# Kernel optimization log

Hardware: AMD Instinct MI355X
Metric: run time of the kernel (lower is better)

The kernel has to match this reference:

```python
import jax, jax.numpy as jnp
import numpy as np

TEMPERATURE = 0.07  # module init default
CHUNK = 2048        # row tile size, mirrors the triton tiling (never materialize full NxN)


def _normalize(x):
    # F.normalize(x, dim=1): x / max(||x||_2, eps)
    n = jnp.linalg.norm(x, axis=1, keepdims=True)
    return x / jnp.maximum(n, 1e-12)


def setup_inputs() -> dict:
    key = jax.random.key(0)
    k1, k2 = jax.random.split(key)
    N, D = 16384, 256
    return {
        "text_features": jax.random.normal(k1, (N, D), dtype=jnp.float32),
        "image_features": jax.random.normal(k2, (N, D), dtype=jnp.float32),
    }


def reference(text_features, image_features):
    X = _normalize(text_features)   # [N, D]
    Y = _normalize(image_features)  # [N, D]
    inv_t = 1.0 / TEMPERATURE
    n, d = X.shape
    Xc = X.reshape(n // CHUNK, CHUNK, d)

    def row_sum_exp(xc):
        # exp2(S*log2(e)/t - log2(e)/t) == exp((S - 1)/t); S = xc @ Y^T
        S = (jnp.einsum('id,jd->ij', xc, Y) - 1.0) * inv_t  # [CHUNK, N]
        return jnp.sum(jnp.exp(S), axis=1)                   # [CHUNK]

    # tiled accumulation of row-wise sum of exponentials (never holds NxN)
    sum_exp_row = jax.lax.map(row_sum_exp, Xc).reshape(n)   # [N]

    # diagonal (positive-pair) logits: Sv = (x_i . y_i - 1)/t
    Sv = (jnp.sum(X * Y, axis=1) - 1.0) * inv_t
    logits = jnp.log(jnp.exp(Sv) / sum_exp_row)
    return -jnp.mean(logits)
```

## Files before the change

### kernel.cpp

```cpp
#include <hip/hip_runtime.h>
#include <hip/hip_bf16.h>
#include <stdint.h>

#define D_DIM 256
#define INV_T 14.285714285714286f

#define BM 256
#define BN 256
#define BK 64
#define NSTEP (D_DIM / BK)

typedef __bf16 bf16x8 __attribute__((ext_vector_type(8)));
typedef float f32x16 __attribute__((ext_vector_type(16)));

__global__ __launch_bounds__(256) void lit_normalize(
    const float* __restrict__ X, const float* __restrict__ Y,
    __hip_bfloat16* __restrict__ Xb, __hip_bfloat16* __restrict__ Yb,
    float* __restrict__ Sv, float* __restrict__ rowsum, float* __restrict__ acc1)
{
    const int l = threadIdx.x & 63;
    const int row = blockIdx.x * 4 + (threadIdx.x >> 6);
    const size_t base = (size_t)row * D_DIM;
    const float4 x = ((const float4*)(X + base))[l];
    const float4 y = ((const float4*)(Y + base))[l];
    float nx = x.x * x.x + x.y * x.y + x.z * x.z + x.w * x.w;
    float ny = y.x * y.x + y.y * y.y + y.z * y.z + y.w * y.w;
    float dt = x.x * y.x + x.y * y.y + x.z * y.z + x.w * y.w;
    #pragma unroll
    for (int o = 1; o < 64; o <<= 1) {
        nx += __shfl_xor(nx, o);
        ny += __shfl_xor(ny, o);
        dt += __shfl_xor(dt, o);
    }
    const float ivx = 1.0f / fmaxf(sqrtf(nx), 1e-12f);
    const float ivy = 1.0f / fmaxf(sqrtf(ny), 1e-12f);

    __hip_bfloat16 hx0 = __float2bfloat16(x.x * ivx), hx1 = __float2bfloat16(x.y * ivx);
    __hip_bfloat16 hx2 = __float2bfloat16(x.z * ivx), hx3 = __float2bfloat16(x.w * ivx);
    __hip_bfloat16 hy0 = __float2bfloat16(y.x * ivy), hy1 = __float2bfloat16(y.y * ivy);
    __hip_bfloat16 hy2 = __float2bfloat16(y.z * ivy), hy3 = __float2bfloat16(y.w * ivy);
    ushort4 px, py;
    px.x = *(unsigned short*)&hx0; px.y = *(unsigned short*)&hx1;
    px.z = *(unsigned short*)&hx2; px.w = *(unsigned short*)&hx3;
    py.x = *(unsigned short*)&hy0; py.y = *(unsigned short*)&hy1;
    py.z = *(unsigned short*)&hy2; py.w = *(unsigned short*)&hy3;
    ((ushort4*)(Xb + base))[l] = px;
    ((ushort4*)(Yb + base))[l] = py;

    if (l == 0) {
        Sv[row] = (dt * ivx * ivy - 1.0f) * INV_T;
        rowsum[row] = 0.0f;
    }
    if (blockIdx.x == 0 && threadIdx.x == 0) acc1[0] = 0.0f;
}

__global__ __launch_bounds__(512, 2) void lit_gemm_rowsum(
    const __hip_bfloat16* __restrict__ Xb, const __hip_bfloat16* __restrict__ Yb,
    float* __restrict__ rowsum)
{
    __shared__ char lds[BM * BK * 2 + BN * BK * 2];

    const int tid = (int)threadIdx.x;
    const int l   = tid & 63;
    const int w   = tid >> 6;
    const int wi  = w >> 2;
    const int wj  = w & 3;

    const int nx  = (int)gridDim.x;
    const int bid = (int)blockIdx.y * nx + (int)blockIdx.x;
    const int cpx = (nx * (int)gridDim.y) >> 3;
    const int logical = (bid & 7) * cpx + (bid >> 3);
    const int bi = logical / nx;
    const int bj = logical % nx;
    const int iBase = bi * BM;
    const int jBase = bj * BN;

    f32x16 acc[2][4];
    #pragma unroll
    for (int a = 0; a < 2; ++a)
        #pragma unroll
        for (int b = 0; b < 4; ++b)
            #pragma unroll
            for (int r = 0; r < 16; ++r)
                acc[a][b][r] = 0.f;

    const int rq = l >> 3;
    const int sl = l & 7;
    const char* src[8];
    int dst[8];
    #pragma unroll
    for (int c = 0; c < 8; ++c) {
        const int g    = w * 8 + c;
        const int isY  = g >> 5;
        const int r8   = (g & 31) * 8;
        const int row  = r8 + rq;
        const int slot = sl ^ (row & 7);
        const char* base = isY ? (const char*)Yb + (size_t)jBase * (D_DIM * 2)
                               : (const char*)Xb + (size_t)iBase * (D_DIM * 2);
        src[c] = base + (size_t)row * (D_DIM * 2) + slot * 16;
        dst[c] = isY * (BM * BK * 2) + r8 * 128;
    }

    #pragma unroll
    for (int t = 0; t < NSTEP; ++t) {
        #pragma unroll
        for (int c = 0; c < 8; ++c)
            __builtin_amdgcn_global_load_lds(
                (const __attribute__((address_space(1))) void*)(src[c] + t * (BK * 2)),
                (__attribute__((address_space(3))) void*)(lds + dst[c]),
                16, 0, 0);
        __syncthreads();

        const char* Xs = lds;
        const char* Ys = lds + BM * BK * 2;
        #pragma unroll
        for (int kk = 0; kk < 4; ++kk) {
            const int sx = ((kk * 2 + (l >> 5)) ^ (l & 7)) * 16;
            const int lr = l & 31;
            bf16x8 a0 = *(const bf16x8*)(Ys + (wj * 64 +  0 + lr) * 128 + sx);
            bf16x8 a1 = *(const bf16x8*)(Ys + (wj * 64 + 32 + lr) * 128 + sx);
            bf16x8 b0 = *(const bf16x8*)(Xs + (wi * 128 +  0 + lr) * 128 + sx);
            bf16x8 b1 = *(const bf16x8*)(Xs + (wi * 128 + 32 + lr) * 128 + sx);
            bf16x8 b2 = *(const bf16x8*)(Xs + (wi * 128 + 64 + lr) * 128 + sx);
            bf16x8 b3 = *(const bf16x8*)(Xs + (wi * 128 + 96 + lr) * 128 + sx);
            acc[0][0] = __builtin_amdgcn_mfma_f32_32x32x16_bf16(a0, b0, acc[0][0], 0, 0, 0);
            acc[0][1] = __builtin_amdgcn_mfma_f32_32x32x16_bf16(a0, b1, acc[0][1], 0, 0, 0);
            acc[0][2] = __builtin_amdgcn_mfma_f32_32x32x16_bf16(a0, b2, acc[0][2], 0, 0, 0);
            acc[0][3] = __builtin_amdgcn_mfma_f32_32x32x16_bf16(a0, b3, acc[0][3], 0, 0, 0);
            acc[1][0] = __builtin_amdgcn_mfma_f32_32x32x16_bf16(a1, b0, acc[1][0], 0, 0, 0);
            acc[1][1] = __builtin_amdgcn_mfma_f32_32x32x16_bf16(a1, b1, acc[1][1], 0, 0, 0);
            acc[1][2] = __builtin_amdgcn_mfma_f32_32x32x16_bf16(a1, b2, acc[1][2], 0, 0, 0);
            acc[1][3] = __builtin_amdgcn_mfma_f32_32x32x16_bf16(a1, b3, acc[1][3], 0, 0, 0);
        }
        __syncthreads();
    }

    float part[4];
    #pragma unroll
    for (int fi = 0; fi < 4; ++fi) {
        float s = 0.f;
        #pragma unroll
        for (int fj = 0; fj < 2; ++fj)
            #pragma unroll
            for (int r = 0; r < 16; ++r)
                s += __expf(fmaf(acc[fj][fi][r], INV_T, -INV_T));
        s += __shfl_xor(s, 32);
        part[fi] = s;
    }
    float* rowpart = (float*)lds;
    if (tid < BM) rowpart[tid] = 0.f;
    __syncthreads();
    if (l < 32) {
        #pragma unroll
        for (int fi = 0; fi < 4; ++fi)
            atomicAdd(&rowpart[wi * 128 + fi * 32 + l], part[fi]);
    }
    __syncthreads();
    if (tid < BM) atomicAdd(&rowsum[iBase + tid], rowpart[tid]);
}

__global__ __launch_bounds__(256) void lit_partial(
    const float* __restrict__ Sv, const float* __restrict__ rowsum,
    float* __restrict__ acc1)
{
    const int i = blockIdx.x * 256 + threadIdx.x;
    float v = Sv[i] - logf(rowsum[i]);
    #pragma unroll
    for (int o = 1; o < 64; o <<= 1) v += __shfl_xor(v, o);
    __shared__ float sred[4];
    if ((threadIdx.x & 63) == 0) sred[threadIdx.x >> 6] = v;
    __syncthreads();
    if (threadIdx.x == 0)
        atomicAdd(acc1, sred[0] + sred[1] + sred[2] + sred[3]);
}

__global__ void lit_final(const float* __restrict__ acc1, float* __restrict__ out, int N)
{
    out[0] = -acc1[0] / (float)N;
}

extern "C" void kernel_launch(void* const* d_in, const int* in_sizes, int n_in,
                              void* d_out, int out_size, void* d_ws, size_t ws_size,
                              hipStream_t stream)
{
    const float* X = (const float*)d_in[0];
    const float* Y = (const float*)d_in[1];
    const int N = in_sizes[0] / D_DIM;

    char* ws = (char*)d_ws;
    __hip_bfloat16* Xb = (__hip_bfloat16*)ws;
    __hip_bfloat16* Yb = (__hip_bfloat16*)(ws + (size_t)N * D_DIM * 2);
    float* Sv     = (float*)(ws + (size_t)N * D_DIM * 4);
    float* rowsum = (float*)(ws + (size_t)N * D_DIM * 4 + (size_t)N * 4);
    float* acc1   = (float*)(ws + (size_t)N * D_DIM * 4 + (size_t)N * 8);

    lit_normalize<<<N / 4, 256, 0, stream>>>(X, Y, Xb, Yb, Sv, rowsum, acc1);
    dim3 grid(N / BN, N / BM);
    lit_gemm_rowsum<<<grid, 512, 0, stream>>>(Xb, Yb, rowsum);
    lit_partial<<<N / 256, 256, 0, stream>>>(Sv, rowsum, acc1);
    lit_final<<<1, 1, 0, stream>>>(acc1, (float*)d_out, N);
}
```

Measured before the change: 265.5 us.

## Double-buffer GEMM K tiles with async LDS loads and fuse final reduction

Cuts the K tile to 32 and double-buffers LDS so the global-to-LDS load of the next tile overlaps the MFMAs on the current one, using explicit vmcnt waits and raw barriers, with a new swizzle for the 64-byte rows. It raises wave priority around the MFMA bursts. It also drops the partial and final kernels by having the last finishing GEMM block, found through an atomic counter, compute the log-sum mean. This saves two launches but adds a serial tail reduction done by one block.

```diff
diff --git a/kernel.cpp b/kernel.cpp
--- a/kernel.cpp
+++ b/kernel.cpp
@@ -7,7 +7,7 @@
 
 #define BM 256
 #define BN 256
-#define BK 64
+#define BK 32
 #define NSTEP (D_DIM / BK)
 
 typedef __bf16 bf16x8 __attribute__((ext_vector_type(8)));
@@ -16,7 +16,7 @@
 __global__ __launch_bounds__(256) void lit_normalize(
     const float* __restrict__ X, const float* __restrict__ Y,
     __hip_bfloat16* __restrict__ Xb, __hip_bfloat16* __restrict__ Yb,
-    float* __restrict__ Sv, float* __restrict__ rowsum, float* __restrict__ acc1)
+    float* __restrict__ Sv, float* __restrict__ rowsum, unsigned* __restrict__ done)
 {
     const int l = threadIdx.x & 63;
     const int row = blockIdx.x * 4 + (threadIdx.x >> 6);
@@ -51,14 +51,15 @@
         Sv[row] = (dt * ivx * ivy - 1.0f) * INV_T;
         rowsum[row] = 0.0f;
     }
-    if (blockIdx.x == 0 && threadIdx.x == 0) acc1[0] = 0.0f;
+    if (blockIdx.x == 0 && threadIdx.x == 0) done[0] = 0u;
 }
 
 __global__ __launch_bounds__(512, 2) void lit_gemm_rowsum(
     const __hip_bfloat16* __restrict__ Xb, const __hip_bfloat16* __restrict__ Yb,
-    float* __restrict__ rowsum)
+    const float* __restrict__ Sv, float* __restrict__ rowsum,
+    unsigned* __restrict__ done, float* __restrict__ out, int N)
 {
-    __shared__ char lds[BM * BK * 2 + BN * BK * 2];
+    __shared__ char lds[2 * 32768];
 
     const int tid = (int)threadIdx.x;
     const int l   = tid & 63;
@@ -84,45 +85,59 @@
             for (int r = 0; r < 16; ++r)
                 acc[a][b][r] = 0.f;
 
-    const int rq = l >> 3;
-    const int sl = l & 7;
-    const char* src[8];
-    int dst[8];
-    #pragma unroll
-    for (int c = 0; c < 8; ++c) {
-        const int g    = w * 8 + c;
-        const int isY  = g >> 5;
-        const int r8   = (g & 31) * 8;
-        const int row  = r8 + rq;
-        const int slot = sl ^ (row & 7);
+    const int rq = l >> 2;
+    const int sl = l & 3;
+    const char* src[4];
+    int dst[4];
+    #pragma unroll
+    for (int c = 0; c < 4; ++c) {
+        const int g    = w * 4 + c;
+        const int isY  = g >> 4;
+        const int r16  = (g & 15) * 16;
+        const int row  = r16 + rq;
+        const int slot = sl ^ ((row >> 1) & 3);
         const char* base = isY ? (const char*)Yb + (size_t)jBase * (D_DIM * 2)
                                : (const char*)Xb + (size_t)iBase * (D_DIM * 2);
         src[c] = base + (size_t)row * (D_DIM * 2) + slot * 16;
-        dst[c] = isY * (BM * BK * 2) + r8 * 128;
-    }
+        dst[c] = isY * 16384 + r16 * 64;
+    }
+
+#define STAGE(buf, t)                                                              \
+    {                                                                              \
+        _Pragma("unroll")                                                          \
+        for (int c = 0; c < 4; ++c)                                                \
+            __builtin_amdgcn_global_load_lds(                                      \
+                (const __attribute__((address_space(1))) void*)(src[c] + (t) * (BK * 2)), \
+                (__attribute__((address_space(3))) void*)(lds + (buf) * 32768 + dst[c]),  \
+                16, 0, 0);                                                         \
+    }
+
+    STAGE(0, 0);
 
     #pragma unroll
     for (int t = 0; t < NSTEP; ++t) {
-        #pragma unroll
-        for (int c = 0; c < 8; ++c)
-            __builtin_amdgcn_global_load_lds(
-                (const __attribute__((address_space(1))) void*)(src[c] + t * (BK * 2)),
-                (__attribute__((address_space(3))) void*)(lds + dst[c]),
-                16, 0, 0);
-        __syncthreads();
-
-        const char* Xs = lds;
-        const char* Ys = lds + BM * BK * 2;
-        #pragma unroll
-        for (int kk = 0; kk < 4; ++kk) {
-            const int sx = ((kk * 2 + (l >> 5)) ^ (l & 7)) * 16;
-            const int lr = l & 31;
-            bf16x8 a0 = *(const bf16x8*)(Ys + (wj * 64 +  0 + lr) * 128 + sx);
-            bf16x8 a1 = *(const bf16x8*)(Ys + (wj * 64 + 32 + lr) * 128 + sx);
-            bf16x8 b0 = *(const bf16x8*)(Xs + (wi * 128 +  0 + lr) * 128 + sx);
-            bf16x8 b1 = *(const bf16x8*)(Xs + (wi * 128 + 32 + lr) * 128 + sx);
-            bf16x8 b2 = *(const bf16x8*)(Xs + (wi * 128 + 64 + lr) * 128 + sx);
-            bf16x8 b3 = *(const bf16x8*)(Xs + (wi * 128 + 96 + lr) * 128 + sx);
+        if (t < NSTEP - 1) {
+            STAGE((t + 1) & 1, t + 1);
+            asm volatile("s_waitcnt vmcnt(4)" ::: "memory");
+        } else {
+            asm volatile("s_waitcnt vmcnt(0)" ::: "memory");
+        }
+        __builtin_amdgcn_sched_barrier(0);
+        __builtin_amdgcn_s_barrier();
+
+        const char* Xs = lds + (t & 1) * 32768;
+        const char* Ys = Xs + 16384;
+        const int lr = l & 31;
+        #pragma unroll
+        for (int kk = 0; kk < 2; ++kk) {
+            const int sx = ((kk * 2 + (l >> 5)) ^ ((l >> 1) & 3)) * 16;
+            bf16x8 a0 = *(const bf16x8*)(Ys + (wj * 64 +  0 + lr) * 64 + sx);
+            bf16x8 a1 = *(const bf16x8*)(Ys + (wj * 64 + 32 + lr) * 64 + sx);
+            bf16x8 b0 = *(const bf16x8*)(Xs + (wi * 128 +  0 + lr) * 64 + sx);
+            bf16x8 b1 = *(const bf16x8*)(Xs + (wi * 128 + 32 + lr) * 64 + sx);
+            bf16x8 b2 = *(const bf16x8*)(Xs + (wi * 128 + 64 + lr) * 64 + sx);
+            bf16x8 b3 = *(const bf16x8*)(Xs + (wi * 128 + 96 + lr) * 64 + sx);
+            __builtin_amdgcn_s_setprio(1);
             acc[0][0] = __builtin_amdgcn_mfma_f32_32x32x16_bf16(a0, b0, acc[0][0], 0, 0, 0);
             acc[0][1] = __builtin_amdgcn_mfma_f32_32x32x16_bf16(a0, b1, acc[0][1], 0, 0, 0);
             acc[0][2] = __builtin_amdgcn_mfma_f32_32x32x16_bf16(a0, b2, acc[0][2], 0, 0, 0);
@@ -131,8 +146,10 @@
             acc[1][1] = __builtin_amdgcn_mfma_f32_32x32x16_bf16(a1, b1, acc[1][1], 0, 0, 0);
             acc[1][2] = __builtin_amdgcn_mfma_f32_32x32x16_bf16(a1, b2, acc[1][2], 0, 0, 0);
             acc[1][3] = __builtin_amdgcn_mfma_f32_32x32x16_bf16(a1, b3, acc[1][3], 0, 0, 0);
-        }
-        __syncthreads();
+            __builtin_amdgcn_s_setprio(0);
+        }
+        __builtin_amdgcn_sched_barrier(0);
+        __builtin_amdgcn_s_barrier();
     }
 
     float part[4];
@@ -157,26 +174,34 @@
     }
     __syncthreads();
     if (tid < BM) atomicAdd(&rowsum[iBase + tid], rowpart[tid]);
-}
-
-__global__ __launch_bounds__(256) void lit_partial(
-    const float* __restrict__ Sv, const float* __restrict__ rowsum,
-    float* __restrict__ acc1)
-{
-    const int i = blockIdx.x * 256 + threadIdx.x;
-    float v = Sv[i] - logf(rowsum[i]);
-    #pragma unroll
-    for (int o = 1; o < 64; o <<= 1) v += __shfl_xor(v, o);
-    __shared__ float sred[4];
-    if ((threadIdx.x & 63) == 0) sred[threadIdx.x >> 6] = v;
-    __syncthreads();
-    if (threadIdx.x == 0)
-        atomicAdd(acc1, sred[0] + sred[1] + sred[2] + sred[3]);
-}
-
-__global__ void lit_final(const float* __restrict__ acc1, float* __restrict__ out, int N)
-{
-    out[0] = -acc1[0] / (float)N;
+
+    __threadfence();
+    __syncthreads();
+    __shared__ unsigned lastBlock;
+    if (tid == 0) {
+        unsigned old = atomicAdd(done, 1u);
+        lastBlock = (old == (unsigned)(gridDim.x * gridDim.y) - 1u) ? 1u : 0u;
+        if (lastBlock) __threadfence();
+    }
+    __syncthreads();
+    if (lastBlock) {
+        float s = 0.f;
+        for (int r = tid; r < N; r += 512) {
+            float rs = __hip_atomic_load(&rowsum[r], __ATOMIC_RELAXED, __HIP_MEMORY_SCOPE_AGENT);
+            s += Sv[r] - __logf(rs);
+        }
+        #pragma unroll
+        for (int o = 1; o < 64; o <<= 1) s += __shfl_xor(s, o);
+        __shared__ float fr[8];
+        if ((tid & 63) == 0) fr[tid >> 6] = s;
+        __syncthreads();
+        if (tid == 0) {
+            float tot = 0.f;
+            #pragma unroll
+            for (int k = 0; k < 8; ++k) tot += fr[k];
+            out[0] = -tot / (float)N;
+        }
+    }
 }
 
 extern "C" void kernel_launch(void* const* d_in, const int* in_sizes, int n_in,
@@ -190,13 +215,11 @@
     char* ws = (char*)d_ws;
     __hip_bfloat16* Xb = (__hip_bfloat16*)ws;
     __hip_bfloat16* Yb = (__hip_bfloat16*)(ws + (size_t)N * D_DIM * 2);
-    float* Sv     = (float*)(ws + (size_t)N * D_DIM * 4);
-    float* rowsum = (float*)(ws + (size_t)N * D_DIM * 4 + (size_t)N * 4);
-    float* acc1   = (float*)(ws + (size_t)N * D_DIM * 4 + (size_t)N * 8);
-
-    lit_normalize<<<N / 4, 256, 0, stream>>>(X, Y, Xb, Yb, Sv, rowsum, acc1);
+    float* Sv       = (float*)(ws + (size_t)N * D_DIM * 4);
+    float* rowsum   = (float*)(ws + (size_t)N * D_DIM * 4 + (size_t)N * 4);
+    unsigned* done  = (unsigned*)(ws + (size_t)N * D_DIM * 4 + (size_t)N * 8);
+
+    lit_normalize<<<N / 4, 256, 0, stream>>>(X, Y, Xb, Yb, Sv, rowsum, done);
     dim3 grid(N / BN, N / BM);
-    lit_gemm_rowsum<<<grid, 512, 0, stream>>>(Xb, Yb, rowsum);
-    lit_partial<<<N / 256, 256, 0, stream>>>(Sv, rowsum, acc1);
-    lit_final<<<1, 1, 0, stream>>>(acc1, (float*)d_out, N);
+    lit_gemm_rowsum<<<grid, 512, 0, stream>>>(Xb, Yb, Sv, rowsum, done, (float*)d_out, N);
 }
```

Measured after the change: 764.5 us. +187.9%, slower.
